# Kernel tuning notes

Hardware: AMD Instinct MI355X
Metric: run time of the kernel (lower is better)

Reference implementation:

```python
import jax, jax.numpy as jnp
import numpy as np

B, L, D, H, S = 16, 512, 512, 16, 3
FF = 4 * D
DH = D // H
EPS = 1e-5


def _bn(x, g, b):
    # BatchNorm1d in training mode: x is (B, C, L); biased variance over (B, L).
    m = jnp.mean(x, axis=(0, 2), keepdims=True)
    v = jnp.var(x, axis=(0, 2), keepdims=True)
    return (x - m) * jax.lax.rsqrt(v + EPS) * g[None, :, None] + b[None, :, None]


def setup_inputs() -> dict:
    key = jax.random.key(0)
    ks = jax.random.split(key, 8)
    s = 0.05
    return {
        "x": jax.random.normal(ks[0], (B, L, D), jnp.float32),
        "emb": jax.random.normal(ks[1], (D, D), jnp.float32) * s,  # emb[0], (in, out); hidden==input_dim
        "bn2_g": jnp.ones((D,), jnp.float32),
        "bn2_b": jnp.zeros((D,), jnp.float32),
        "Wq": jax.random.normal(ks[2], (S, D, D), jnp.float32) * s,  # stored (in,out)
        "bq": jnp.zeros((S, D), jnp.float32),
        "Wk": jax.random.normal(ks[3], (S, D, D), jnp.float32) * s,
        "bk": jnp.zeros((S, D), jnp.float32),
        "Wv": jax.random.normal(ks[4], (S, D, D), jnp.float32) * s,
        "bv": jnp.zeros((S, D), jnp.float32),
        "bna_g": jnp.ones((S, D), jnp.float32),
        "bna_b": jnp.zeros((S, D), jnp.float32),
        "W1": jax.random.normal(ks[5], (S, D, FF), jnp.float32) * s,  # conv1 1x1, (in,out)
        "b1": jnp.zeros((S, FF), jnp.float32),
        "W2": jax.random.normal(ks[6], (S, FF, D), jnp.float32) * s,  # conv2 1x1, (in,out)
        "b2": jnp.zeros((S, D), jnp.float32),
        "bnf_g": jnp.ones((S, D), jnp.float32),
        "bnf_b": jnp.zeros((S, D), jnp.float32),
    }


def _split_heads(t):
    # torch.cat(torch.split(t, D//H, dim=2), dim=0): (B,L,D) -> (H*B, L, DH), head-major on dim0.
    return jnp.moveaxis(t.reshape(B, L, H, DH), 2, 0).reshape(H * B, L, DH)


def reference(x, emb, bn2_g, bn2_b, Wq, bq, Wk, bk, Wv, bv, bna_g, bna_b,
              W1, b1, W2, b2, bnf_g, bnf_b):
    scale = 1.0 / np.sqrt(DH).astype(np.float32)
    xp = jnp.swapaxes(x, 1, 2)                      # (B, D, L)
    enc = jnp.einsum('bil,io->bol', xp, emb)        # 1x1 conv embedding, no bias
    enc = _bn(enc, bn2_g, bn2_b)                    # (B, D, L)
    for i in range(S):
        xin = jnp.swapaxes(enc, 1, 2)               # (B, L, D)
        Q = jax.nn.relu(xin @ Wq[i] + bq[i])
        K = jax.nn.relu(xin @ Wk[i] + bk[i])
        V = jax.nn.relu(xin @ Wv[i] + bv[i])
        Q_, K_, V_ = _split_heads(Q), _split_heads(K), _split_heads(V)  # (H*B, L, DH)
        sc = jnp.einsum('nqd,nkd->nqk', Q_, K_) * scale                 # (H*B, L, L)
        att = jax.nn.softmax(sc, axis=0)            # softmax over batch*heads dim (as in source)
        o = jnp.einsum('nqk,nkd->nqd', att, V_)     # (H*B, L, DH)
        # torch.cat(torch.split(o, B, dim=0), dim=2): (H*B,L,DH) -> (B,L,D)
        o = o.reshape(H, B, L, DH).transpose(1, 2, 0, 3).reshape(B, L, D)
        o = o + xin
        enc = _bn(jnp.swapaxes(o, 1, 2), bna_g[i], bna_b[i])            # (B, D, L)
        # FeedForward: 1x1 conv -> relu -> 1x1 conv -> residual -> BN
        h1 = jax.nn.relu(jnp.einsum('bdl,df->bfl', enc, W1[i]) + b1[i][None, :, None])
        h2 = jnp.einsum('bfl,fd->bdl', h1, W2[i]) + b2[i][None, :, None]
        enc = _bn(h2 + enc, bnf_g[i], bnf_b[i])
    return jnp.swapaxes(enc, 1, 2)                  # (B, L, D)
```

## Files before the change

kernel.cpp:

```cpp
#include <hip/hip_runtime.h>

#define DEVI __device__ __forceinline__

typedef unsigned short u16;
typedef __attribute__((ext_vector_type(8))) short s16x8;
typedef __attribute__((ext_vector_type(4))) float f32x4;
typedef __attribute__((ext_vector_type(4))) unsigned short u16x4v;
typedef __attribute__((ext_vector_type(2))) unsigned int u32x2;

constexpr int NB   = 16;
constexpr int LL   = 512;
constexpr int DD   = 512;
constexpr int FF_  = 2048;
constexpr int NROW = NB * LL;
constexpr float C2 = 0.17677669529663687f * 1.4426950408889634f;
constexpr size_t QKVOFF = (size_t)NROW * DD;

DEVI u16 f2b(float f) {
  unsigned int u = __float_as_uint(f);
  unsigned int r = u + 0x7FFFu + ((u >> 16) & 1u);
  return (u16)(r >> 16);
}

DEVI void gload16(const void* g, void* l) {
  __builtin_amdgcn_global_load_lds(
      (const __attribute__((address_space(1))) unsigned int*)(unsigned long long)g,
      (__attribute__((address_space(3))) unsigned int*)(unsigned int)(unsigned long long)l,
      16, 0, 0);
}

__global__ __launch_bounds__(256) void k_f32_to_bf16(const float* __restrict__ X, u16* __restrict__ Y, int n4) {
  for (int i = blockIdx.x * 256 + threadIdx.x; i < n4; i += gridDim.x * 256) {
    float4 x = ((const float4*)X)[i];
    u16x4v o; o[0] = f2b(x.x); o[1] = f2b(x.y); o[2] = f2b(x.z); o[3] = f2b(x.w);
    ((u16x4v*)Y)[i] = o;
  }
}

__global__ __launch_bounds__(256) void k_zero(float* __restrict__ p, int n) {
  int i = blockIdx.x * 256 + threadIdx.x;
  if (i < n) p[i] = 0.f;
}

__global__ __launch_bounds__(256) void k_recip(float* __restrict__ p, int n) {
  int i = blockIdx.x * 256 + threadIdx.x;
  if (i < n) p[i] = 1.0f / p[i];
}

__global__ void k_catbias(const float* __restrict__ a, const float* __restrict__ b,
                          const float* __restrict__ c, float* __restrict__ o) {
  int i = blockIdx.x * 256 + threadIdx.x;
  o[i] = (i < 512) ? a[i] : (i < 1024) ? b[i - 512] : c[i - 1024];
}

__global__ __launch_bounds__(256) void k_wtrans(const float* __restrict__ W, u16* __restrict__ WT, int K, int M) {
  __shared__ float tile[32][33];
  const int k0 = blockIdx.x * 32, m0 = blockIdx.y * 32;
  const int tx = threadIdx.x & 31, ty = threadIdx.x >> 5;
#pragma unroll
  for (int j = 0; j < 4; ++j) tile[ty + j * 8][tx] = W[(size_t)(k0 + ty + j * 8) * M + m0 + tx];
  __syncthreads();
#pragma unroll
  for (int j = 0; j < 4; ++j) WT[(size_t)(m0 + ty + j * 8) * K + k0 + tx] = f2b(tile[tx][ty + j * 8]);
}

template <int BM, int RELU, int HASB, int HASRES, int OUTF, int OUTB, int STATS, int SPLIT3>
__global__ __launch_bounds__(256) void k_gemm(const u16* __restrict__ A, const u16* __restrict__ Bt,
                                              const float* __restrict__ bias, const float* __restrict__ Res,
                                              float* __restrict__ Cf, u16* __restrict__ Cb,
                                              float* __restrict__ stats, int K, int Ncols) {
  constexpr int WR = BM / 64;
  constexpr int WC = 4 / WR;
  constexpr int MW = 4;
  constexpr int NW = 128 / (16 * WC);
  __shared__ __align__(16) u16 As[BM * 64];
  __shared__ __align__(16) u16 Bs[128 * 64];
  const int t = threadIdx.x, lane = t & 63, w = t >> 6;
  const int wr = w / WC, wc = w % WC, l16 = lane & 15, lhi = lane >> 4;
  const int row0 = blockIdx.x * BM, col0 = blockIdx.y * 128;
  const int sr = lane >> 3, sc = (lane & 7) * 8;
  const u16* Ag = A + (size_t)(row0 + sr) * K + sc;
  const u16* Bg = Bt + (size_t)(col0 + sr) * K + sc;

  f32x4 acc[MW][NW] = {};

  for (int k0 = 0; k0 < K; k0 += 64) {
    __syncthreads();
#pragma unroll
    for (int j = 0; j < BM / 32; ++j) {
      const int ch = w * (BM / 32) + j;
      gload16(Ag + (size_t)(ch * 8) * K + k0, As + ch * 512);
    }
#pragma unroll
    for (int j = 0; j < 4; ++j) {
      const int ch = w * 4 + j;
      gload16(Bg + (size_t)(ch * 8) * K + k0, Bs + ch * 512);
    }
    __syncthreads();
#pragma unroll
    for (int kk = 0; kk < 2; ++kk) {
      s16x8 af[MW], bfv[NW];
#pragma unroll
      for (int m = 0; m < MW; ++m) af[m] = *(const s16x8*)(As + (wr * 64 + m * 16 + l16) * 64 + kk * 32 + lhi * 8);
#pragma unroll
      for (int n = 0; n < NW; ++n) bfv[n] = *(const s16x8*)(Bs + (wc * (16 * NW) + n * 16 + l16) * 64 + kk * 32 + lhi * 8);
#pragma unroll
      for (int m = 0; m < MW; ++m)
#pragma unroll
        for (int n = 0; n < NW; ++n)
          acc[m][n] = __builtin_amdgcn_mfma_f32_16x16x32_bf16(af[m], bfv[n], acc[m][n], 0, 0, 0);
    }
  }

#pragma unroll
  for (int n = 0; n < NW; ++n) {
    const int col = col0 + wc * (16 * NW) + n * 16 + l16;
    float bv = 0.f;
    if constexpr (HASB) bv = bias[col];
    float ssum = 0.f, ssq = 0.f;
#pragma unroll
    for (int m = 0; m < MW; ++m) {
      const int rbase = row0 + wr * 64 + m * 16 + lhi * 4;
#pragma unroll
      for (int r = 0; r < 4; ++r) {
        float v = acc[m][n][r] + bv;
        if constexpr (RELU) v = fmaxf(v, 0.f);
        const int row = rbase + r;
        const size_t idx = (size_t)row * Ncols + col;
        if constexpr (HASRES) v += Res[idx];
        if constexpr (OUTF) Cf[idx] = v;
        if constexpr (OUTB) {
          if constexpr (SPLIT3) {
            const size_t ib = (size_t)(col >> 9) * QKVOFF + (size_t)row * DD + (col & 511);
            Cb[ib] = f2b(v);
          } else {
            Cb[idx] = f2b(v);
          }
        }
        if constexpr (STATS) { ssum += v; ssq += v * v; }
      }
    }
    if constexpr (STATS) {
      ssum += __shfl_xor(ssum, 16); ssq += __shfl_xor(ssq, 16);
      ssum += __shfl_xor(ssum, 32); ssq += __shfl_xor(ssq, 32);
      if (lhi == 0) {
        atomicAdd(&stats[col], ssum);
        atomicAdd(&stats[512 + col], ssq);
      }
    }
  }
}

__global__ __launch_bounds__(256) void k_attn_z(const u16* __restrict__ Q, const u16* __restrict__ Kt,
                                                float* __restrict__ Z) {
  const int t = threadIdx.x, lane = t & 63, w = t >> 6;
  const int l16 = lane & 15, lhi = lane >> 4;
  const int q0 = blockIdx.x * 64 + (w >> 1) * 32;
  const int k0 = blockIdx.y * 64 + (w & 1) * 32;
  const int n0 = blockIdx.z * 16;
  f32x4 zac[2][2] = {};
  for (int nn = 0; nn < 16; ++nn) {
    const int n = n0 + nn, h = n >> 4, b = n & 15;
    const size_t base = (size_t)b * LL * DD + (size_t)h * 32;
    s16x8 a[2], bb[2];
#pragma unroll
    for (int mi = 0; mi < 2; ++mi) a[mi] = *(const s16x8*)(Q + base + (size_t)(q0 + mi * 16 + l16) * DD + lhi * 8);
#pragma unroll
    for (int ni = 0; ni < 2; ++ni) bb[ni] = *(const s16x8*)(Kt + base + (size_t)(k0 + ni * 16 + l16) * DD + lhi * 8);
#pragma unroll
    for (int mi = 0; mi < 2; ++mi)
#pragma unroll
      for (int ni = 0; ni < 2; ++ni) {
        f32x4 z4 = {0.f, 0.f, 0.f, 0.f};
        f32x4 s = __builtin_amdgcn_mfma_f32_16x16x32_bf16(a[mi], bb[ni], z4, 0, 0, 0);
#pragma unroll
        for (int r = 0; r < 4; ++r) zac[mi][ni][r] += exp2f(s[r] * C2);
      }
  }
#pragma unroll
  for (int mi = 0; mi < 2; ++mi)
#pragma unroll
    for (int ni = 0; ni < 2; ++ni)
#pragma unroll
      for (int r = 0; r < 4; ++r)
        atomicAdd(&Z[(q0 + mi * 16 + lhi * 4 + r) * LL + k0 + ni * 16 + l16], zac[mi][ni][r]);
}

__global__ __launch_bounds__(512) void k_attn_pv3(const u16* __restrict__ Q, const u16* __restrict__ K,
                                                  const u16* __restrict__ V, const float* __restrict__ IZ,
                                                  const float* __restrict__ Res, float* __restrict__ T,
                                                  float* __restrict__ stats) {
  __shared__ __align__(16) u16 Kl[512 * 40];
  __shared__ __align__(16) u16 Vl[32 * 520];
  __shared__ __align__(16) u16 Pl[8][1024];
  const int n = blockIdx.x, h = n >> 4, b = n & 15;
  const int t = threadIdx.x, lane = t & 63, w = t >> 6;
  const int l16 = lane & 15, lhi = lane >> 4;
  const size_t base = (size_t)b * LL * DD + (size_t)h * 32;

#pragma unroll
  for (int j = 0; j < 4; ++j) {
    const int c = t + j * 512;
    const int k = c >> 2, part = c & 3;
    const s16x8 v = *(const s16x8*)(K + base + (size_t)k * DD + part * 8);
    *(s16x8*)(Kl + k * 40 + part * 8) = v;
  }
#pragma unroll
  for (int j = 0; j < 4; ++j) {
    const int c = t + j * 512;
    const int k = c >> 2, dp = c & 3;
    const s16x8 v = *(const s16x8*)(V + base + (size_t)k * DD + dp * 8);
#pragma unroll
    for (int jj = 0; jj < 8; ++jj) Vl[(dp * 8 + jj) * 520 + k] = (u16)v[jj];
  }
  const int qbase = w * 64;
  s16x8 aqv[4];
#pragma unroll
  for (int qf = 0; qf < 4; ++qf)
    aqv[qf] = *(const s16x8*)(Q + base + (size_t)(qbase + qf * 16 + l16) * DD + lhi * 8);
  __syncthreads();

  char* P = (char*)&Pl[w][0];
  const int wxor = (l16 & 7) << 4;
  const int wbase = l16 * 128 + lhi * 8;
  float ssum[2] = {0.f, 0.f}, ssq[2] = {0.f, 0.f};

#pragma unroll
  for (int qf = 0; qf < 4; ++qf) {
    const int q16 = qbase + qf * 16;
    const float* izrow = IZ + (size_t)(q16 + l16) * LL + lhi * 4;
    f32x4 oa[2] = {};
#pragma unroll
    for (int kt = 0; kt < 8; ++kt) {
      const int kb = kt * 64;
      f32x4 s[4]; float4 iz[4];
#pragma unroll
      for (int ks = 0; ks < 4; ++ks) {
        const s16x8 af = *(const s16x8*)(Kl + (kb + ks * 16 + l16) * 40 + lhi * 8);
        f32x4 z4 = {0.f, 0.f, 0.f, 0.f};
        s[ks] = __builtin_amdgcn_mfma_f32_16x16x32_bf16(af, aqv[qf], z4, 0, 0, 0);
        iz[ks] = *(const float4*)(izrow + kb + ks * 16);
      }
#pragma unroll
      for (int ks = 0; ks < 4; ++ks) {
        const float p0 = exp2f(s[ks][0] * C2) * iz[ks].x;
        const float p1 = exp2f(s[ks][1] * C2) * iz[ks].y;
        const float p2 = exp2f(s[ks][2] * C2) * iz[ks].z;
        const float p3 = exp2f(s[ks][3] * C2) * iz[ks].w;
        unsigned int pk0, pk1;
        asm("v_cvt_pk_bf16_f32 %0, %1, %2" : "=v"(pk0) : "v"(p0), "v"(p1));
        asm("v_cvt_pk_bf16_f32 %0, %1, %2" : "=v"(pk1) : "v"(p2), "v"(p3));
        u32x2 pw; pw[0] = pk0; pw[1] = pk1;
        *(u32x2*)(P + ((wbase + ks * 32) ^ wxor)) = pw;
      }
#pragma unroll
      for (int kc = 0; kc < 2; ++kc) {
        const s16x8 pa = *(const s16x8*)(P + ((l16 * 128 + kc * 64 + lhi * 16) ^ wxor));
#pragma unroll
        for (int dt = 0; dt < 2; ++dt) {
          const s16x8 bv = *(const s16x8*)(Vl + (dt * 16 + l16) * 520 + kb + kc * 32 + lhi * 8);
          oa[dt] = __builtin_amdgcn_mfma_f32_16x16x32_bf16(pa, bv, oa[dt], 0, 0, 0);
        }
      }
    }
#pragma unroll
    for (int dt = 0; dt < 2; ++dt)
#pragma unroll
      for (int r = 0; r < 4; ++r) {
        const size_t idx = (size_t)(b * LL + q16 + lhi * 4 + r) * DD + h * 32 + dt * 16 + l16;
        const float v = oa[dt][r] + Res[idx];
        T[idx] = v;
        ssum[dt] += v; ssq[dt] += v * v;
      }
  }
#pragma unroll
  for (int dt = 0; dt < 2; ++dt) {
    float su = ssum[dt], sq = ssq[dt];
    su += __shfl_xor(su, 16); sq += __shfl_xor(sq, 16);
    su += __shfl_xor(su, 32); sq += __shfl_xor(sq, 32);
    if (lhi == 0) {
      const int col = h * 32 + dt * 16 + l16;
      atomicAdd(&stats[col], su);
      atomicAdd(&stats[512 + col], sq);
    }
  }
}

__global__ void k_bn_fin(float* __restrict__ S, const float* __restrict__ g,
                         const float* __restrict__ be, float* __restrict__ coef) {
  const int d = threadIdx.x;
  const float inv = 1.0f / 8192.0f;
  const float mean = S[d] * inv;
  const float var = S[512 + d] * inv - mean * mean;
  const float a = rsqrtf(var + 1e-5f) * g[d];
  coef[d] = a;
  coef[512 + d] = be[d] - mean * a;
  S[d] = 0.f; S[512 + d] = 0.f;
}

template <int WB>
__global__ __launch_bounds__(256) void k_bn_apply(const float* __restrict__ X, const float* __restrict__ coef,
                                                  float* __restrict__ Yf, u16* __restrict__ Yb) {
  const int n4 = NROW * DD / 4;
  for (int i = blockIdx.x * 256 + threadIdx.x; i < n4; i += gridDim.x * 256) {
    const float4 xv = ((const float4*)X)[i];
    const int d = (i & 127) * 4;
    const float y0 = fmaf(xv.x, coef[d + 0], coef[512 + d + 0]);
    const float y1 = fmaf(xv.y, coef[d + 1], coef[512 + d + 1]);
    const float y2 = fmaf(xv.z, coef[d + 2], coef[512 + d + 2]);
    const float y3 = fmaf(xv.w, coef[d + 3], coef[512 + d + 3]);
    ((float4*)Yf)[i] = make_float4(y0, y1, y2, y3);
    if constexpr (WB) {
      u16x4v o; o[0] = f2b(y0); o[1] = f2b(y1); o[2] = f2b(y2); o[3] = f2b(y3);
      ((u16x4v*)Yb)[i] = o;
    }
  }
}

extern "C" void kernel_launch(void* const* d_in, const int* in_sizes, int n_in,
                              void* d_out, int out_size, void* d_ws, size_t ws_size,
                              hipStream_t stream) {
  const float* x    = (const float*)d_in[0];
  const float* emb  = (const float*)d_in[1];
  const float* bn2g = (const float*)d_in[2];
  const float* bn2b = (const float*)d_in[3];
  const float* Wq   = (const float*)d_in[4];
  const float* bq   = (const float*)d_in[5];
  const float* Wk   = (const float*)d_in[6];
  const float* bkp  = (const float*)d_in[7];
  const float* Wv   = (const float*)d_in[8];
  const float* bvp  = (const float*)d_in[9];
  const float* bnag = (const float*)d_in[10];
  const float* bnab = (const float*)d_in[11];
  const float* W1   = (const float*)d_in[12];
  const float* b1   = (const float*)d_in[13];
  const float* W2   = (const float*)d_in[14];
  const float* b2   = (const float*)d_in[15];
  const float* bnfg = (const float*)d_in[16];
  const float* bnfb = (const float*)d_in[17];

  char* p = (char*)d_ws;
  auto alloc = [&](size_t bytes) { char* r = p; p += (bytes + 255) & ~(size_t)255; return r; };
  u16*   xb    = (u16*)alloc((size_t)NROW * DD * 2);
  float* encF  = (float*)alloc((size_t)NROW * DD * 4);
  u16*   encB  = (u16*)alloc((size_t)NROW * DD * 2);
  float* tF    = (float*)alloc((size_t)NROW * DD * 4);
  u16*   qkv   = (u16*)alloc((size_t)3 * NROW * DD * 2);
  u16*   h1    = (u16*)alloc((size_t)NROW * FF_ * 2);
  float* Z     = (float*)alloc((size_t)LL * LL * 4);
  float* sums  = (float*)alloc(1024 * 4);
  float* coef  = (float*)alloc(1024 * 4);
  float* bqkv  = (float*)alloc(1536 * 4);
  u16*   embT  = (u16*)alloc((size_t)DD * DD * 2);
  u16*   wqkvT = (u16*)alloc((size_t)3 * DD * DD * 2);
  u16*   w1T   = (u16*)alloc((size_t)DD * FF_ * 2);
  u16*   w2T   = (u16*)alloc((size_t)FF_ * DD * 2);
  if ((size_t)(p - (char*)d_ws) > ws_size) return;

  auto run_bn = [&](const float* Xs, const float* g, const float* be, float* Yf, u16* Yb) {
    k_bn_fin<<<1, 512, 0, stream>>>(sums, g, be, coef);
    if (Yb) k_bn_apply<1><<<2048, 256, 0, stream>>>(Xs, coef, Yf, Yb);
    else    k_bn_apply<0><<<2048, 256, 0, stream>>>(Xs, coef, Yf, nullptr);
  };

  k_zero<<<4, 256, 0, stream>>>(sums, 1024);
  k_f32_to_bf16<<<2048, 256, 0, stream>>>(x, xb, NROW * DD / 4);
  k_wtrans<<<dim3(16, 16), 256, 0, stream>>>(emb, embT, DD, DD);
  k_gemm<128, 0, 0, 0, 1, 0, 1, 0><<<dim3(64, 4), 256, 0, stream>>>(xb, embT, nullptr, nullptr, tF, nullptr, sums, DD, DD);
  run_bn(tF, bn2g, bn2b, encF, encB);

  for (int i = 0; i < 3; ++i) {
    k_wtrans<<<dim3(16, 16), 256, 0, stream>>>(Wq + (size_t)i * DD * DD, wqkvT, DD, DD);
    k_wtrans<<<dim3(16, 16), 256, 0, stream>>>(Wk + (size_t)i * DD * DD, wqkvT + (size_t)512 * DD, DD, DD);
    k_wtrans<<<dim3(16, 16), 256, 0, stream>>>(Wv + (size_t)i * DD * DD, wqkvT + (size_t)1024 * DD, DD, DD);
    k_catbias<<<6, 256, 0, stream>>>(bq + i * DD, bkp + i * DD, bvp + i * DD, bqkv);
    k_gemm<128, 1, 1, 0, 0, 1, 0, 1><<<dim3(64, 12), 256, 0, stream>>>(encB, wqkvT, bqkv, nullptr, nullptr, qkv, nullptr, DD, 1536);
    k_zero<<<1024, 256, 0, stream>>>(Z, LL * LL);
    k_attn_z<<<dim3(8, 8, 16), 256, 0, stream>>>(qkv, qkv + QKVOFF, Z);
    k_recip<<<1024, 256, 0, stream>>>(Z, LL * LL);
    k_attn_pv3<<<256, 512, 0, stream>>>(qkv, qkv + QKVOFF, qkv + 2 * QKVOFF, Z, encF, tF, sums);
    run_bn(tF, bnag + i * DD, bnab + i * DD, encF, encB);
    k_wtrans<<<dim3(16, 64), 256, 0, stream>>>(W1 + (size_t)i * DD * FF_, w1T, DD, FF_);
    k_gemm<128, 1, 1, 0, 0, 1, 0, 0><<<dim3(64, 16), 256, 0, stream>>>(encB, w1T, b1 + i * FF_, nullptr, nullptr, h1, nullptr, DD, FF_);
    k_wtrans<<<dim3(64, 16), 256, 0, stream>>>(W2 + (size_t)i * FF_ * DD, w2T, FF_, DD);
    k_gemm<128, 0, 1, 1, 1, 0, 1, 0><<<dim3(64, 4), 256, 0, stream>>>(h1, w2T, b2 + i * DD, encF, tF, nullptr, sums, FF_, DD);
    float* yf = (i == 2) ? (float*)d_out : encF;
    run_bn(tF, bnfg + i * DD, bnfb + i * DD, yf, (i == 2) ? nullptr : encB);
  }
}
```

Baseline: 717.4 us.

## Recompute BN residual from pre-norm buffer instead of storing fp32 normalized copy

Drops the fp32 normalized activation buffer (encF). Consumers that need the residual now read the un-normalized pre-BN tensor tF and apply the BN affine coefficients on the fly, in both the attention PV epilogue and the FFN second GEMM. BN apply kernels now write only bf16, or fp32 only for the final output, which removes a large fp32 write and read per BN. Separately, the N=512 GEMMs switch to BM=64 tiles for more blocks; this also lets tF be read and written in place, which is why the __restrict__ qualifiers are dropped.

Measured after the change: 673.6 us. 6.1% less time.

```diff
diff --git a/kernel.cpp b/kernel.cpp
--- a/kernel.cpp
+++ b/kernel.cpp
@@ -64,10 +64,11 @@
   for (int j = 0; j < 4; ++j) WT[(size_t)(m0 + ty + j * 8) * K + k0 + tx] = f2b(tile[tx][ty + j * 8]);
 }
 
-template <int BM, int RELU, int HASB, int HASRES, int OUTF, int OUTB, int STATS, int SPLIT3>
+template <int BM, int RELU, int HASB, int HASRES, int RESBN, int OUTF, int OUTB, int STATS, int SPLIT3>
 __global__ __launch_bounds__(256) void k_gemm(const u16* __restrict__ A, const u16* __restrict__ Bt,
-                                              const float* __restrict__ bias, const float* __restrict__ Res,
-                                              float* __restrict__ Cf, u16* __restrict__ Cb,
+                                              const float* __restrict__ bias, const float* Res,
+                                              const float* __restrict__ resco,
+                                              float* Cf, u16* __restrict__ Cb,
                                               float* __restrict__ stats, int K, int Ncols) {
   constexpr int WR = BM / 64;
   constexpr int WC = 4 / WR;
@@ -117,6 +118,8 @@
     const int col = col0 + wc * (16 * NW) + n * 16 + l16;
     float bv = 0.f;
     if constexpr (HASB) bv = bias[col];
+    float ra = 0.f, rc = 0.f;
+    if constexpr (RESBN) { ra = resco[col]; rc = resco[512 + col]; }
     float ssum = 0.f, ssq = 0.f;
 #pragma unroll
     for (int m = 0; m < MW; ++m) {
@@ -127,7 +130,10 @@
         if constexpr (RELU) v = fmaxf(v, 0.f);
         const int row = rbase + r;
         const size_t idx = (size_t)row * Ncols + col;
-        if constexpr (HASRES) v += Res[idx];
+        if constexpr (HASRES) {
+          if constexpr (RESBN) v += fmaf(Res[idx], ra, rc);
+          else v += Res[idx];
+        }
         if constexpr (OUTF) Cf[idx] = v;
         if constexpr (OUTB) {
           if constexpr (SPLIT3) {
@@ -188,7 +194,7 @@
 
 __global__ __launch_bounds__(512) void k_attn_pv3(const u16* __restrict__ Q, const u16* __restrict__ K,
                                                   const u16* __restrict__ V, const float* __restrict__ IZ,
-                                                  const float* __restrict__ Res, float* __restrict__ T,
+                                                  const float* __restrict__ resco, float* T,
                                                   float* __restrict__ stats) {
   __shared__ __align__(16) u16 Kl[512 * 40];
   __shared__ __align__(16) u16 Vl[32 * 520];
@@ -218,6 +224,12 @@
 #pragma unroll
   for (int qf = 0; qf < 4; ++qf)
     aqv[qf] = *(const s16x8*)(Q + base + (size_t)(qbase + qf * 16 + l16) * DD + lhi * 8);
+  float ra[2], rc[2];
+#pragma unroll
+  for (int dt = 0; dt < 2; ++dt) {
+    const int col = h * 32 + dt * 16 + l16;
+    ra[dt] = resco[col]; rc[dt] = resco[512 + col];
+  }
   __syncthreads();
 
   char* P = (char*)&Pl[w][0];
@@ -268,7 +280,7 @@
 #pragma unroll
       for (int r = 0; r < 4; ++r) {
         const size_t idx = (size_t)(b * LL + q16 + lhi * 4 + r) * DD + h * 32 + dt * 16 + l16;
-        const float v = oa[dt][r] + Res[idx];
+        const float v = oa[dt][r] + fmaf(T[idx], ra[dt], rc[dt]);
         T[idx] = v;
         ssum[dt] += v; ssq[dt] += v * v;
       }
@@ -298,22 +310,33 @@
   S[d] = 0.f; S[512 + d] = 0.f;
 }
 
-template <int WB>
-__global__ __launch_bounds__(256) void k_bn_apply(const float* __restrict__ X, const float* __restrict__ coef,
-                                                  float* __restrict__ Yf, u16* __restrict__ Yb) {
+__global__ __launch_bounds__(256) void k_bn_applyB(const float* __restrict__ X, const float* __restrict__ coef,
+                                                   u16* __restrict__ Yb) {
   const int n4 = NROW * DD / 4;
   for (int i = blockIdx.x * 256 + threadIdx.x; i < n4; i += gridDim.x * 256) {
     const float4 xv = ((const float4*)X)[i];
     const int d = (i & 127) * 4;
-    const float y0 = fmaf(xv.x, coef[d + 0], coef[512 + d + 0]);
-    const float y1 = fmaf(xv.y, coef[d + 1], coef[512 + d + 1]);
-    const float y2 = fmaf(xv.z, coef[d + 2], coef[512 + d + 2]);
-    const float y3 = fmaf(xv.w, coef[d + 3], coef[512 + d + 3]);
-    ((float4*)Yf)[i] = make_float4(y0, y1, y2, y3);
-    if constexpr (WB) {
-      u16x4v o; o[0] = f2b(y0); o[1] = f2b(y1); o[2] = f2b(y2); o[3] = f2b(y3);
-      ((u16x4v*)Yb)[i] = o;
-    }
+    u16x4v o;
+    o[0] = f2b(fmaf(xv.x, coef[d + 0], coef[512 + d + 0]));
+    o[1] = f2b(fmaf(xv.y, coef[d + 1], coef[512 + d + 1]));
+    o[2] = f2b(fmaf(xv.z, coef[d + 2], coef[512 + d + 2]));
+    o[3] = f2b(fmaf(xv.w, coef[d + 3], coef[512 + d + 3]));
+    ((u16x4v*)Yb)[i] = o;
+  }
+}
+
+__global__ __launch_bounds__(256) void k_bn_applyF(const float* __restrict__ X, const float* __restrict__ coef,
+                                                   float* __restrict__ Yf) {
+  const int n4 = NROW * DD / 4;
+  for (int i = blockIdx.x * 256 + threadIdx.x; i < n4; i += gridDim.x * 256) {
+    const float4 xv = ((const float4*)X)[i];
+    const int d = (i & 127) * 4;
+    float4 o;
+    o.x = fmaf(xv.x, coef[d + 0], coef[512 + d + 0]);
+    o.y = fmaf(xv.y, coef[d + 1], coef[512 + d + 1]);
+    o.z = fmaf(xv.z, coef[d + 2], coef[512 + d + 2]);
+    o.w = fmaf(xv.w, coef[d + 3], coef[512 + d + 3]);
+    ((float4*)Yf)[i] = o;
   }
 }
 
@@ -342,7 +365,6 @@
   char* p = (char*)d_ws;
   auto alloc = [&](size_t bytes) { char* r = p; p += (bytes + 255) & ~(size_t)255; return r; };
   u16*   xb    = (u16*)alloc((size_t)NROW * DD * 2);
-  float* encF  = (float*)alloc((size_t)NROW * DD * 4);
   u16*   encB  = (u16*)alloc((size_t)NROW * DD * 2);
   float* tF    = (float*)alloc((size_t)NROW * DD * 4);
   u16*   qkv   = (u16*)alloc((size_t)3 * NROW * DD * 2);
@@ -357,34 +379,35 @@
   u16*   w2T   = (u16*)alloc((size_t)FF_ * DD * 2);
   if ((size_t)(p - (char*)d_ws) > ws_size) return;
 
-  auto run_bn = [&](const float* Xs, const float* g, const float* be, float* Yf, u16* Yb) {
-    k_bn_fin<<<1, 512, 0, stream>>>(sums, g, be, coef);
-    if (Yb) k_bn_apply<1><<<2048, 256, 0, stream>>>(Xs, coef, Yf, Yb);
-    else    k_bn_apply<0><<<2048, 256, 0, stream>>>(Xs, coef, Yf, nullptr);
-  };
-
   k_zero<<<4, 256, 0, stream>>>(sums, 1024);
   k_f32_to_bf16<<<2048, 256, 0, stream>>>(x, xb, NROW * DD / 4);
   k_wtrans<<<dim3(16, 16), 256, 0, stream>>>(emb, embT, DD, DD);
-  k_gemm<128, 0, 0, 0, 1, 0, 1, 0><<<dim3(64, 4), 256, 0, stream>>>(xb, embT, nullptr, nullptr, tF, nullptr, sums, DD, DD);
-  run_bn(tF, bn2g, bn2b, encF, encB);
+  k_gemm<64, 0, 0, 0, 0, 1, 0, 1, 0><<<dim3(128, 4), 256, 0, stream>>>(
+      xb, embT, nullptr, nullptr, nullptr, tF, nullptr, sums, DD, DD);
+  k_bn_fin<<<1, 512, 0, stream>>>(sums, bn2g, bn2b, coef);
+  k_bn_applyB<<<2048, 256, 0, stream>>>(tF, coef, encB);
 
   for (int i = 0; i < 3; ++i) {
     k_wtrans<<<dim3(16, 16), 256, 0, stream>>>(Wq + (size_t)i * DD * DD, wqkvT, DD, DD);
     k_wtrans<<<dim3(16, 16), 256, 0, stream>>>(Wk + (size_t)i * DD * DD, wqkvT + (size_t)512 * DD, DD, DD);
     k_wtrans<<<dim3(16, 16), 256, 0, stream>>>(Wv + (size_t)i * DD * DD, wqkvT + (size_t)1024 * DD, DD, DD);
     k_catbias<<<6, 256, 0, stream>>>(bq + i * DD, bkp + i * DD, bvp + i * DD, bqkv);
-    k_gemm<128, 1, 1, 0, 0, 1, 0, 1><<<dim3(64, 12), 256, 0, stream>>>(encB, wqkvT, bqkv, nullptr, nullptr, qkv, nullptr, DD, 1536);
+    k_gemm<128, 1, 1, 0, 0, 0, 1, 0, 1><<<dim3(64, 12), 256, 0, stream>>>(
+        encB, wqkvT, bqkv, nullptr, nullptr, nullptr, qkv, nullptr, DD, 1536);
     k_zero<<<1024, 256, 0, stream>>>(Z, LL * LL);
     k_attn_z<<<dim3(8, 8, 16), 256, 0, stream>>>(qkv, qkv + QKVOFF, Z);
     k_recip<<<1024, 256, 0, stream>>>(Z, LL * LL);
-    k_attn_pv3<<<256, 512, 0, stream>>>(qkv, qkv + QKVOFF, qkv + 2 * QKVOFF, Z, encF, tF, sums);
-    run_bn(tF, bnag + i * DD, bnab + i * DD, encF, encB);
+    k_attn_pv3<<<256, 512, 0, stream>>>(qkv, qkv + QKVOFF, qkv + 2 * QKVOFF, Z, coef, tF, sums);
+    k_bn_fin<<<1, 512, 0, stream>>>(sums, bnag + i * DD, bnab + i * DD, coef);
+    k_bn_applyB<<<2048, 256, 0, stream>>>(tF, coef, encB);
     k_wtrans<<<dim3(16, 64), 256, 0, stream>>>(W1 + (size_t)i * DD * FF_, w1T, DD, FF_);
-    k_gemm<128, 1, 1, 0, 0, 1, 0, 0><<<dim3(64, 16), 256, 0, stream>>>(encB, w1T, b1 + i * FF_, nullptr, nullptr, h1, nullptr, DD, FF_);
+    k_gemm<128, 1, 1, 0, 0, 0, 1, 0, 0><<<dim3(64, 16), 256, 0, stream>>>(
+        encB, w1T, b1 + i * FF_, nullptr, nullptr, nullptr, h1, nullptr, DD, FF_);
     k_wtrans<<<dim3(64, 16), 256, 0, stream>>>(W2 + (size_t)i * FF_ * DD, w2T, FF_, DD);
-    k_gemm<128, 0, 1, 1, 1, 0, 1, 0><<<dim3(64, 4), 256, 0, stream>>>(h1, w2T, b2 + i * DD, encF, tF, nullptr, sums, FF_, DD);
-    float* yf = (i == 2) ? (float*)d_out : encF;
-    run_bn(tF, bnfg + i * DD, bnfb + i * DD, yf, (i == 2) ? nullptr : encB);
-  }
-}
+    k_gemm<64, 0, 1, 1, 1, 1, 0, 1, 0><<<dim3(128, 4), 256, 0, stream>>>(
+        h1, w2T, b2 + i * DD, tF, coef, tF, nullptr, sums, FF_, DD);
+    k_bn_fin<<<1, 512, 0, stream>>>(sums, bnfg + i * DD, bnfb + i * DD, coef);
+    if (i == 2) k_bn_applyF<<<2048, 256, 0, stream>>>(tF, coef, (float*)d_out);
+    else        k_bn_applyB<<<2048, 256, 0, stream>>>(tF, coef, encB);
+  }
+}
```
